# Performance work log

Measured on AMD Instinct MI355X. Metric: run time of the kernel, lower is better.

The kernel has to match this reference:

```python
import jax, jax.numpy as jnp
import numpy as np

N = 100000      # nodes
E = 1600000     # edges (before self-loops)
IN = 128        # in_channels
H = 4           # heads
C = 32          # hidden_channels (per head)
HC = H * C      # 128, LayerNorm dim
NEG_SLOPE = 0.2
LN_EPS = 1e-5


def setup_inputs() -> dict:
    key = jax.random.key(0)
    ks = jax.random.split(key, 8)
    x = jax.random.normal(ks[0], (N, IN), dtype=jnp.float32)
    edge_index = jax.random.randint(ks[1], (2, E), 0, N, dtype=jnp.int64)
    edge_weight = jax.random.uniform(ks[2], (E,), dtype=jnp.float32)
    # GATConv parameters
    W = jax.random.normal(ks[3], (IN, HC), dtype=jnp.float32) * (1.0 / np.sqrt(IN))
    att_src = jax.random.normal(ks[4], (H, C), dtype=jnp.float32) * (1.0 / np.sqrt(C))
    att_dst = jax.random.normal(ks[5], (H, C), dtype=jnp.float32) * (1.0 / np.sqrt(C))
    bias = jnp.zeros((HC,), dtype=jnp.float32)
    # LayerNorm parameters
    gamma = jnp.ones((HC,), dtype=jnp.float32)
    beta = jnp.zeros((HC,), dtype=jnp.float32)
    return {"x": x, "edge_index": edge_index, "edge_weight": edge_weight,
            "W": W, "att_src": att_src, "att_dst": att_dst, "bias": bias,
            "gamma": gamma, "beta": beta}


def reference(x, edge_index, edge_weight, W, att_src, att_dst, bias, gamma, beta):
    # --- GATConv (heads=4, concat, add_self_loops=True) ---
    loops = jnp.arange(N, dtype=edge_index.dtype)
    ei = jnp.concatenate([edge_index, jnp.stack([loops, loops])], axis=1)  # [2, E+N]
    src, dst = ei[0], ei[1]

    xw = (x @ W).reshape(N, H, C)                       # [N, H, C]
    a_src = jnp.sum(xw * att_src, axis=-1)              # [N, H]
    a_dst = jnp.sum(xw * att_dst, axis=-1)              # [N, H]

    # per-edge attention logits, softmax grouped by destination node
    e = jax.nn.leaky_relu(a_src[src] + a_dst[dst], NEG_SLOPE)   # [E+N, H]
    m = jax.ops.segment_max(e, dst, num_segments=N)             # [N, H]
    ex = jnp.exp(e - m[dst])
    denom = jax.ops.segment_sum(ex, dst, num_segments=N)        # [N, H]
    alpha = ex / (denom[dst] + 1e-16)                           # [E+N, H]

    # weighted scatter-add of source features to destinations
    msg = alpha[:, :, None] * xw[src]                           # [E+N, H, C]
    out = jax.ops.segment_sum(msg, dst, num_segments=N)         # [N, H, C]
    out = out.reshape(N, HC) + bias                             # concat heads + bias

    # --- LayerNorm ---
    mu = jnp.mean(out, axis=-1, keepdims=True)
    var = jnp.var(out, axis=-1, keepdims=True)
    return gamma * (out - mu) / jnp.sqrt(var + LN_EPS) + beta
```

## Files before the change

kernel.cpp:

```cpp
#include <hip/hip_runtime.h>
#include <math.h>

#define NN 100000
#define EE 1600000
#define ETOT (EE + NN)
#define NBUK 512
#define NPB 196
#define CHUNK 3125
#define CAP 6144

typedef __attribute__((ext_vector_type(8))) short bf16x8;
typedef __attribute__((ext_vector_type(4))) float f32x4;

__device__ __forceinline__ unsigned short f2bf(float f) {
  unsigned int u = __float_as_uint(f);
  u = u + 0x7fffu + ((u >> 16) & 1u);
  return (unsigned short)(u >> 16);
}

__device__ __forceinline__ float lrelu_exp(float e) {
  e = (e > 0.f) ? e : 0.2f * e;
  return __expf(e);
}

__global__ __launch_bounds__(256) void k_gemm(const float* __restrict__ x,
                                              const float* __restrict__ W,
                                              const float* __restrict__ att_src,
                                              const float* __restrict__ att_dst,
                                              unsigned short* __restrict__ xwb,
                                              float* __restrict__ asrc,
                                              float* __restrict__ adst) {
  __shared__ __align__(16) unsigned short lds[17408];
  __shared__ float satt[256];
  int tid = threadIdx.x;
  for (int i = tid; i < 16384; i += 256) {
    int k = i >> 7, n = i & 127;
    lds[n * 136 + k] = f2bf(W[i]);
  }
  if (tid < 128) satt[tid] = att_src[tid];
  else satt[tid] = att_dst[tid - 128];
  __syncthreads();

  int wv = tid >> 6, lane = tid & 63;
  int m = lane & 15, q = lane >> 4;
  int r = blockIdx.x * 64 + wv * 16 + m;
  bool rok = (r < NN);

  bf16x8 af[4];
#pragma unroll
  for (int kt = 0; kt < 4; kt++) {
    float4 v0 = make_float4(0.f, 0.f, 0.f, 0.f), v1 = v0;
    if (rok) {
      v0 = ((const float4*)x)[(size_t)r * 32 + kt * 8 + q * 2];
      v1 = ((const float4*)x)[(size_t)r * 32 + kt * 8 + q * 2 + 1];
    }
    af[kt][0] = (short)f2bf(v0.x); af[kt][1] = (short)f2bf(v0.y);
    af[kt][2] = (short)f2bf(v0.z); af[kt][3] = (short)f2bf(v0.w);
    af[kt][4] = (short)f2bf(v1.x); af[kt][5] = (short)f2bf(v1.y);
    af[kt][6] = (short)f2bf(v1.z); af[kt][7] = (short)f2bf(v1.w);
  }

  f32x4 acc[8];
#pragma unroll
  for (int nt = 0; nt < 8; nt++) acc[nt] = (f32x4){0.f, 0.f, 0.f, 0.f};

#pragma unroll
  for (int nt = 0; nt < 8; nt++) {
#pragma unroll
    for (int kt = 0; kt < 4; kt++) {
      bf16x8 bf = *((const bf16x8*)&lds[(nt * 16 + m) * 136 + kt * 32 + q * 8]);
      acc[nt] = __builtin_amdgcn_mfma_f32_16x16x32_bf16(af[kt], bf, acc[nt], 0, 0, 0);
    }
  }

  __syncthreads();
#pragma unroll
  for (int nt = 0; nt < 8; nt++)
#pragma unroll
    for (int rg = 0; rg < 4; rg++)
      lds[(wv * 16 + q * 4 + rg) * 128 + nt * 16 + m] = f2bf(acc[nt][rg]);
  __syncthreads();

  size_t base = (size_t)blockIdx.x * 16384;
  const size_t lim = (size_t)NN * 256;
  for (int i = tid; i < 1024; i += 256) {
    size_t off = base + (size_t)i * 16;
    if (off < lim) *((uint4*)((char*)xwb + off)) = ((const uint4*)lds)[i];
  }

  int row = tid >> 2, h = tid & 3;
  int node = blockIdx.x * 64 + row;
  if (node < NN) {
    float ss = 0.f, sd = 0.f;
#pragma unroll
    for (int cq = 0; cq < 4; cq++) {
      uint4 u = *((const uint4*)&lds[row * 128 + h * 32 + cq * 8]);
      int cb = h * 32 + cq * 8;
      float f0 = __uint_as_float(u.x << 16), f1 = __uint_as_float(u.x & 0xffff0000u);
      float f2 = __uint_as_float(u.y << 16), f3 = __uint_as_float(u.y & 0xffff0000u);
      float f4 = __uint_as_float(u.z << 16), f5 = __uint_as_float(u.z & 0xffff0000u);
      float f6 = __uint_as_float(u.w << 16), f7 = __uint_as_float(u.w & 0xffff0000u);
      ss += f0 * satt[cb] + f1 * satt[cb + 1] + f2 * satt[cb + 2] + f3 * satt[cb + 3] +
            f4 * satt[cb + 4] + f5 * satt[cb + 5] + f6 * satt[cb + 6] + f7 * satt[cb + 7];
      sd += f0 * satt[128 + cb] + f1 * satt[128 + cb + 1] + f2 * satt[128 + cb + 2] +
            f3 * satt[128 + cb + 3] + f4 * satt[128 + cb + 4] + f5 * satt[128 + cb + 5] +
            f6 * satt[128 + cb + 6] + f7 * satt[128 + cb + 7];
    }
    asrc[(size_t)node * 4 + h] = ss;
    adst[(size_t)node * 4 + h] = sd;
  }
}

__global__ __launch_bounds__(256) void k_p1(const int* __restrict__ ei,
                                            int* __restrict__ H) {
  __shared__ int h[NBUK];
  int j = blockIdx.x, t = threadIdx.x;
  for (int i = t; i < NBUK; i += 256) h[i] = 0;
  __syncthreads();
  int e0 = j * CHUNK;
  for (int e = e0 + t; e < e0 + CHUNK; e += 256) {
    int d = ei[(size_t)EE + e];
    atomicAdd(&h[d / NPB], 1);
  }
  __syncthreads();
  for (int i = t; i < NBUK; i += 256) H[j * NBUK + i] = h[i];
}

__global__ __launch_bounds__(512) void k_s1(const int* __restrict__ H,
                                            int* __restrict__ R, int* __restrict__ T) {
  __shared__ int s[512];
  int b = blockIdx.x, t = threadIdx.x;
  int v = H[t * NBUK + b];
  s[t] = v;
  __syncthreads();
  for (int off = 1; off < 512; off <<= 1) {
    int tmp = (t >= off) ? s[t - off] : 0;
    __syncthreads();
    s[t] += tmp;
    __syncthreads();
  }
  R[b * 512 + t] = s[t] - v;
  if (t == 511) T[b] = s[511];
}

__global__ __launch_bounds__(512) void k_s2(const int* __restrict__ T,
                                            int* __restrict__ BaseTmp,
                                            int* __restrict__ Base) {
  __shared__ int s[512];
  __shared__ int s2[512];
  int t = threadIdx.x;
  int v = T[t];
  int ncnt = NN - t * NPB;
  ncnt = (ncnt < 0) ? 0 : ((ncnt > NPB) ? NPB : ncnt);
  int w = v + ncnt;
  s[t] = v; s2[t] = w;
  __syncthreads();
  for (int off = 1; off < 512; off <<= 1) {
    int ta = (t >= off) ? s[t - off] : 0;
    int tb = (t >= off) ? s2[t - off] : 0;
    __syncthreads();
    s[t] += ta; s2[t] += tb;
    __syncthreads();
  }
  BaseTmp[t] = s[t] - v;
  Base[t] = s2[t] - w;
}

__global__ __launch_bounds__(256) void k_p3(const int* __restrict__ ei,
                                            const int* __restrict__ R,
                                            const int* __restrict__ BaseTmp,
                                            int* __restrict__ tmpb) {
  __shared__ int cur[NBUK];
  int j = blockIdx.x, t = threadIdx.x;
  for (int b = t; b < NBUK; b += 256) cur[b] = BaseTmp[b] + R[b * 512 + j];
  __syncthreads();
  int e0 = j * CHUNK;
  for (int e = e0 + t; e < e0 + CHUNK; e += 256) {
    int s = ei[e];
    int d = ei[(size_t)EE + e];
    int b = d / NPB;
    int li = d - b * NPB;
    int pos = atomicAdd(&cur[b], 1);
    tmpb[pos] = (li << 17) | s;
  }
}

__global__ __launch_bounds__(256) void k_p4(const int* __restrict__ tmpb,
                                            const int* __restrict__ T,
                                            const int* __restrict__ BaseTmp,
                                            const int* __restrict__ Base,
                                            const float* __restrict__ asrc,
                                            const float* __restrict__ adst,
                                            int* __restrict__ es, int* __restrict__ offs,
                                            float* __restrict__ na) {
  __shared__ int cnt[256];
  __shared__ int cur[NPB];
  __shared__ int stage[CAP];
  __shared__ __align__(16) float ssum[NPB * 4];
  __shared__ __align__(16) float adl[NPB * 4];
  int b = blockIdx.x, t = threadIdx.x;
  if (b == 0 && t == 0) offs[NN] = ETOT;
  int n0 = b * NPB;
  int nloc = NN - n0;
  if (nloc <= 0) return;
  if (nloc > NPB) nloc = NPB;
  int total = T[b];
  int bt = BaseTmp[b], bs = Base[b];
  cnt[t] = (t < nloc) ? 1 : 0;
  for (int i = t; i < NPB * 4; i += 256) ssum[i] = 0.f;
  for (int i = t; i < nloc * 4; i += 256) adl[i] = adst[(size_t)n0 * 4 + i];
  __syncthreads();
  for (int e = t; e < total; e += 256) {
    int u = tmpb[bt + e];
    atomicAdd(&cnt[u >> 17], 1);
  }
  __syncthreads();
  int v = cnt[t];
  __syncthreads();
  for (int off = 1; off < 256; off <<= 1) {
    int tmp = (t >= off) ? cnt[t - off] : 0;
    __syncthreads();
    cnt[t] += tmp;
    __syncthreads();
  }
  int excl = cnt[t] - v;
  if (t < nloc) {
    int node = n0 + t;
    offs[node] = bs + excl;
    cur[t] = excl + 1;
    if (excl < CAP) {
      stage[excl] = node;
      float4 asv = *((const float4*)(asrc + (size_t)node * 4));
      float4 adv = *((const float4*)&adl[t * 4]);
      float4 w4;
      w4.x = lrelu_exp(asv.x + adv.x); w4.y = lrelu_exp(asv.y + adv.y);
      w4.z = lrelu_exp(asv.z + adv.z); w4.w = lrelu_exp(asv.w + adv.w);
      atomicAdd(&ssum[t * 4 + 0], w4.x); atomicAdd(&ssum[t * 4 + 1], w4.y);
      atomicAdd(&ssum[t * 4 + 2], w4.z); atomicAdd(&ssum[t * 4 + 3], w4.w);
    }
  }
  __syncthreads();
  for (int e = t; e < total; e += 256) {
    int u = tmpb[bt + e];
    int li = u >> 17;
    int src = u & 0x1FFFF;
    int pos = atomicAdd(&cur[li], 1);
    if (pos < CAP) {
      stage[pos] = src;
      float4 asv = *((const float4*)(asrc + (size_t)src * 4));
      float4 adv = *((const float4*)&adl[li * 4]);
      float4 w4;
      w4.x = lrelu_exp(asv.x + adv.x); w4.y = lrelu_exp(asv.y + adv.y);
      w4.z = lrelu_exp(asv.z + adv.z); w4.w = lrelu_exp(asv.w + adv.w);
      atomicAdd(&ssum[li * 4 + 0], w4.x); atomicAdd(&ssum[li * 4 + 1], w4.y);
      atomicAdd(&ssum[li * 4 + 2], w4.z); atomicAdd(&ssum[li * 4 + 3], w4.w);
    }
  }
  __syncthreads();
  int btot = total + nloc;
  if (btot > CAP) btot = CAP;
  for (int i = t; i < btot; i += 256) es[bs + i] = stage[i];
  for (int i = t; i < nloc * 4; i += 256)
    na[(size_t)n0 * 4 + i] = 1.f / (ssum[i] + 1e-16f);
}

__global__ __launch_bounds__(256) void k_agg(const unsigned short* __restrict__ xwb,
                                             const float* __restrict__ asrc,
                                             const float* __restrict__ adst,
                                             const float* __restrict__ na,
                                             const int* __restrict__ offs,
                                             const int* __restrict__ es,
                                             const float* __restrict__ bias,
                                             const float* __restrict__ gamma,
                                             const float* __restrict__ beta,
                                             float* __restrict__ out) {
  int lane = threadIdx.x & 63;
  int node = blockIdx.x * 4 + (threadIdx.x >> 6);
  int off0 = offs[node];
  int d = offs[node + 1] - off0;
  int h = lane >> 4;
  int c = lane * 2;
  float rn = na[(size_t)node * 4 + h];
  float ad = adst[(size_t)node * 4 + h];

  const unsigned* xp = (const unsigned*)xwb + lane;
  const int* ep = es + off0;
  float ax0 = 0.f, ay0 = 0.f, ax1 = 0.f, ay1 = 0.f;

  int j = 0;
  for (; j + 8 <= d; j += 8) {
    int4 sa = *((const int4*)(ep + j));
    int4 sb = *((const int4*)(ep + j + 4));
    int sv[8] = {sa.x, sa.y, sa.z, sa.w, sb.x, sb.y, sb.z, sb.w};
    float av[8];
    unsigned uu[8];
#pragma unroll
    for (int q = 0; q < 8; q++) {
      av[q] = asrc[(size_t)(unsigned)sv[q] * 4 + h];
      uu[q] = xp[(unsigned)sv[q] * 64u];
    }
#pragma unroll
    for (int q = 0; q < 8; q++) {
      float w = lrelu_exp(av[q] + ad);
      float lo = __uint_as_float(uu[q] << 16);
      float hi = __uint_as_float(uu[q] & 0xffff0000u);
      if (q & 1) { ax1 = fmaf(w, lo, ax1); ay1 = fmaf(w, hi, ay1); }
      else       { ax0 = fmaf(w, lo, ax0); ay0 = fmaf(w, hi, ay0); }
    }
  }
  for (; j < d; ++j) {
    int s0 = ep[j];
    float w = lrelu_exp(asrc[(size_t)(unsigned)s0 * 4 + h] + ad);
    unsigned u0 = xp[(unsigned)s0 * 64u];
    ax0 = fmaf(w, __uint_as_float(u0 << 16), ax0);
    ay0 = fmaf(w, __uint_as_float(u0 & 0xffff0000u), ay0);
  }
  float accx = ax0 + ax1, accy = ay0 + ay1;

  float vx = accx * rn + bias[c];
  float vy = accy * rn + bias[c + 1];
  float sum = vx + vy, sq = vx * vx + vy * vy;
#pragma unroll
  for (int o = 32; o; o >>= 1) {
    sum += __shfl_xor(sum, o);
    sq += __shfl_xor(sq, o);
  }
  float mean = sum * (1.f / 128.f);
  float var = sq * (1.f / 128.f) - mean * mean;
  float rs = rsqrtf(var + 1e-5f);
  float o0 = gamma[c] * (vx - mean) * rs + beta[c];
  float o1 = gamma[c + 1] * (vy - mean) * rs + beta[c + 1];
  float2 ov; ov.x = o0; ov.y = o1;
  *((float2*)(out + (size_t)node * 128 + c)) = ov;
}

extern "C" void kernel_launch(void* const* d_in, const int* in_sizes, int n_in,
                              void* d_out, int out_size, void* d_ws, size_t ws_size,
                              hipStream_t stream) {
  const float* x = (const float*)d_in[0];
  const int* ei = (const int*)d_in[1];
  const float* W = (const float*)d_in[3];
  const float* att_src = (const float*)d_in[4];
  const float* att_dst = (const float*)d_in[5];
  const float* bias = (const float*)d_in[6];
  const float* gamma = (const float*)d_in[7];
  const float* beta = (const float*)d_in[8];
  float* out = (float*)d_out;

  char* p = (char*)d_ws;
  auto alloc = [&](size_t bytes) -> char* {
    char* r = p;
    p += (bytes + 255) & ~(size_t)255;
    return r;
  };
  unsigned short* xwb = (unsigned short*)alloc((size_t)NN * 128 * 2);
  float* asrc = (float*)alloc((size_t)NN * 4 * 4);
  float* adst = (float*)alloc((size_t)NN * 4 * 4);
  int* es = (int*)alloc((size_t)ETOT * 4);
  int* offs = (int*)alloc((size_t)(NN + 1) * 4);
  float* na = (float*)alloc((size_t)NN * 4 * 4);
  int* tmpb = (int*)alloc((size_t)EE * 4);
  int* H = (int*)alloc((size_t)512 * NBUK * 4);
  int* R = (int*)alloc((size_t)NBUK * 512 * 4);
  int* T = (int*)alloc((size_t)NBUK * 4);
  int* BaseTmp = (int*)alloc((size_t)(NBUK + 1) * 4);
  int* Base = (int*)alloc((size_t)(NBUK + 1) * 4);

  k_gemm<<<(NN + 63) / 64, 256, 0, stream>>>(x, W, att_src, att_dst, xwb, asrc, adst);
  k_p1<<<512, 256, 0, stream>>>(ei, H);
  k_s1<<<NBUK, 512, 0, stream>>>(H, R, T);
  k_s2<<<1, 512, 0, stream>>>(T, BaseTmp, Base);
  k_p3<<<512, 256, 0, stream>>>(ei, R, BaseTmp, tmpb);
  k_p4<<<NBUK, 256, 0, stream>>>(tmpb, T, BaseTmp, Base, asrc, adst, es, offs, na);
  k_agg<<<NN / 4, 256, 0, stream>>>(xwb, asrc, adst, na, offs, es, bias, gamma, beta, out);
}
```

Baseline: 302.6 us.

## Fuse softmax denominator into aggregation and compute edge weights once per lane

The per-destination softmax denominator is no longer computed in the CSR build kernel (k_p4) with shared-memory float atomics. Instead, k_agg accumulates the sum of weights alongside the weighted features and normalises at the end. Inside the 8-edge loop, each lane now computes one (edge, head) exponential and broadcasts it with shuffles, rather than every lane recomputing exp for all 8 edges. This removes the asrc gathers, the exps and the atomics from k_p4, plus the na buffer round trip, in exchange for extra shuffles and a running sum in the aggregation kernel.

After: 270.6 us. 10.6% less time.

```diff
diff --git a/kernel.cpp b/kernel.cpp
--- a/kernel.cpp
+++ b/kernel.cpp
@@ -189,15 +189,10 @@
                                             const int* __restrict__ T,
                                             const int* __restrict__ BaseTmp,
                                             const int* __restrict__ Base,
-                                            const float* __restrict__ asrc,
-                                            const float* __restrict__ adst,
-                                            int* __restrict__ es, int* __restrict__ offs,
-                                            float* __restrict__ na) {
+                                            int* __restrict__ es, int* __restrict__ offs) {
   __shared__ int cnt[256];
   __shared__ int cur[NPB];
   __shared__ int stage[CAP];
-  __shared__ __align__(16) float ssum[NPB * 4];
-  __shared__ __align__(16) float adl[NPB * 4];
   int b = blockIdx.x, t = threadIdx.x;
   if (b == 0 && t == 0) offs[NN] = ETOT;
   int n0 = b * NPB;
@@ -207,8 +202,6 @@
   int total = T[b];
   int bt = BaseTmp[b], bs = Base[b];
   cnt[t] = (t < nloc) ? 1 : 0;
-  for (int i = t; i < NPB * 4; i += 256) ssum[i] = 0.f;
-  for (int i = t; i < nloc * 4; i += 256) adl[i] = adst[(size_t)n0 * 4 + i];
   __syncthreads();
   for (int e = t; e < total; e += 256) {
     int u = tmpb[bt + e];
@@ -225,49 +218,25 @@
   }
   int excl = cnt[t] - v;
   if (t < nloc) {
-    int node = n0 + t;
-    offs[node] = bs + excl;
+    offs[n0 + t] = bs + excl;
     cur[t] = excl + 1;
-    if (excl < CAP) {
-      stage[excl] = node;
-      float4 asv = *((const float4*)(asrc + (size_t)node * 4));
-      float4 adv = *((const float4*)&adl[t * 4]);
-      float4 w4;
-      w4.x = lrelu_exp(asv.x + adv.x); w4.y = lrelu_exp(asv.y + adv.y);
-      w4.z = lrelu_exp(asv.z + adv.z); w4.w = lrelu_exp(asv.w + adv.w);
-      atomicAdd(&ssum[t * 4 + 0], w4.x); atomicAdd(&ssum[t * 4 + 1], w4.y);
-      atomicAdd(&ssum[t * 4 + 2], w4.z); atomicAdd(&ssum[t * 4 + 3], w4.w);
-    }
+    if (excl < CAP) stage[excl] = n0 + t;
   }
   __syncthreads();
   for (int e = t; e < total; e += 256) {
     int u = tmpb[bt + e];
-    int li = u >> 17;
-    int src = u & 0x1FFFF;
-    int pos = atomicAdd(&cur[li], 1);
-    if (pos < CAP) {
-      stage[pos] = src;
-      float4 asv = *((const float4*)(asrc + (size_t)src * 4));
-      float4 adv = *((const float4*)&adl[li * 4]);
-      float4 w4;
-      w4.x = lrelu_exp(asv.x + adv.x); w4.y = lrelu_exp(asv.y + adv.y);
-      w4.z = lrelu_exp(asv.z + adv.z); w4.w = lrelu_exp(asv.w + adv.w);
-      atomicAdd(&ssum[li * 4 + 0], w4.x); atomicAdd(&ssum[li * 4 + 1], w4.y);
-      atomicAdd(&ssum[li * 4 + 2], w4.z); atomicAdd(&ssum[li * 4 + 3], w4.w);
-    }
+    int pos = atomicAdd(&cur[u >> 17], 1);
+    if (pos < CAP) stage[pos] = u & 0x1FFFF;
   }
   __syncthreads();
   int btot = total + nloc;
   if (btot > CAP) btot = CAP;
   for (int i = t; i < btot; i += 256) es[bs + i] = stage[i];
-  for (int i = t; i < nloc * 4; i += 256)
-    na[(size_t)n0 * 4 + i] = 1.f / (ssum[i] + 1e-16f);
 }
 
 __global__ __launch_bounds__(256) void k_agg(const unsigned short* __restrict__ xwb,
                                              const float* __restrict__ asrc,
                                              const float* __restrict__ adst,
-                                             const float* __restrict__ na,
                                              const int* __restrict__ offs,
                                              const int* __restrict__ es,
                                              const float* __restrict__ bias,
@@ -279,43 +248,69 @@
   int off0 = offs[node];
   int d = offs[node + 1] - off0;
   int h = lane >> 4;
+  int he = lane & 3;
   int c = lane * 2;
-  float rn = na[(size_t)node * 4 + h];
-  float ad = adst[(size_t)node * 4 + h];
+
+  float4 ad4 = *((const float4*)(adst + (size_t)node * 4));
+  float adh = (h & 2) ? ((h & 1) ? ad4.w : ad4.z) : ((h & 1) ? ad4.y : ad4.x);
+  float ade = (he & 2) ? ((he & 1) ? ad4.w : ad4.z) : ((he & 1) ? ad4.y : ad4.x);
 
   const unsigned* xp = (const unsigned*)xwb + lane;
   const int* ep = es + off0;
   float ax0 = 0.f, ay0 = 0.f, ax1 = 0.f, ay1 = 0.f;
+  float wsum = 0.f;
 
   int j = 0;
   for (; j + 8 <= d; j += 8) {
     int4 sa = *((const int4*)(ep + j));
     int4 sb = *((const int4*)(ep + j + 4));
-    int sv[8] = {sa.x, sa.y, sa.z, sa.w, sb.x, sb.y, sb.z, sb.w};
-    float av[8];
-    unsigned uu[8];
-#pragma unroll
-    for (int q = 0; q < 8; q++) {
-      av[q] = asrc[(size_t)(unsigned)sv[q] * 4 + h];
-      uu[q] = xp[(unsigned)sv[q] * 64u];
-    }
-#pragma unroll
-    for (int q = 0; q < 8; q++) {
-      float w = lrelu_exp(av[q] + ad);
-      float lo = __uint_as_float(uu[q] << 16);
-      float hi = __uint_as_float(uu[q] & 0xffff0000u);
-      if (q & 1) { ax1 = fmaf(w, lo, ax1); ay1 = fmaf(w, hi, ay1); }
-      else       { ax0 = fmaf(w, lo, ax0); ay0 = fmaf(w, hi, ay0); }
-    }
+    int se = ep[j + (lane >> 3)];
+    float av = asrc[(size_t)(unsigned)se * 4u + (unsigned)he];
+    unsigned u0 = xp[(unsigned)sa.x * 64u];
+    unsigned u1 = xp[(unsigned)sa.y * 64u];
+    unsigned u2 = xp[(unsigned)sa.z * 64u];
+    unsigned u3 = xp[(unsigned)sa.w * 64u];
+    unsigned u4 = xp[(unsigned)sb.x * 64u];
+    unsigned u5 = xp[(unsigned)sb.y * 64u];
+    unsigned u6 = xp[(unsigned)sb.z * 64u];
+    unsigned u7 = xp[(unsigned)sb.w * 64u];
+    float wl = lrelu_exp(av + ade);
+    float w0 = __shfl(wl, 0 * 8 + h);
+    float w1 = __shfl(wl, 1 * 8 + h);
+    float w2 = __shfl(wl, 2 * 8 + h);
+    float w3 = __shfl(wl, 3 * 8 + h);
+    float w4 = __shfl(wl, 4 * 8 + h);
+    float w5 = __shfl(wl, 5 * 8 + h);
+    float w6 = __shfl(wl, 6 * 8 + h);
+    float w7 = __shfl(wl, 7 * 8 + h);
+    wsum += ((w0 + w1) + (w2 + w3)) + ((w4 + w5) + (w6 + w7));
+    ax0 = fmaf(w0, __uint_as_float(u0 << 16), ax0);
+    ay0 = fmaf(w0, __uint_as_float(u0 & 0xffff0000u), ay0);
+    ax1 = fmaf(w1, __uint_as_float(u1 << 16), ax1);
+    ay1 = fmaf(w1, __uint_as_float(u1 & 0xffff0000u), ay1);
+    ax0 = fmaf(w2, __uint_as_float(u2 << 16), ax0);
+    ay0 = fmaf(w2, __uint_as_float(u2 & 0xffff0000u), ay0);
+    ax1 = fmaf(w3, __uint_as_float(u3 << 16), ax1);
+    ay1 = fmaf(w3, __uint_as_float(u3 & 0xffff0000u), ay1);
+    ax0 = fmaf(w4, __uint_as_float(u4 << 16), ax0);
+    ay0 = fmaf(w4, __uint_as_float(u4 & 0xffff0000u), ay0);
+    ax1 = fmaf(w5, __uint_as_float(u5 << 16), ax1);
+    ay1 = fmaf(w5, __uint_as_float(u5 & 0xffff0000u), ay1);
+    ax0 = fmaf(w6, __uint_as_float(u6 << 16), ax0);
+    ay0 = fmaf(w6, __uint_as_float(u6 & 0xffff0000u), ay0);
+    ax1 = fmaf(w7, __uint_as_float(u7 << 16), ax1);
+    ay1 = fmaf(w7, __uint_as_float(u7 & 0xffff0000u), ay1);
   }
   for (; j < d; ++j) {
     int s0 = ep[j];
-    float w = lrelu_exp(asrc[(size_t)(unsigned)s0 * 4 + h] + ad);
+    float w = lrelu_exp(asrc[(size_t)(unsigned)s0 * 4u + (unsigned)h] + adh);
+    wsum += w;
     unsigned u0 = xp[(unsigned)s0 * 64u];
     ax0 = fmaf(w, __uint_as_float(u0 << 16), ax0);
     ay0 = fmaf(w, __uint_as_float(u0 & 0xffff0000u), ay0);
   }
   float accx = ax0 + ax1, accy = ay0 + ay1;
+  float rn = 1.f / (wsum + 1e-16f);
 
   float vx = accx * rn + bias[c];
   float vy = accy * rn + bias[c + 1];
@@ -358,7 +353,6 @@
   float* adst = (float*)alloc((size_t)NN * 4 * 4);
   int* es = (int*)alloc((size_t)ETOT * 4);
   int* offs = (int*)alloc((size_t)(NN + 1) * 4);
-  float* na = (float*)alloc((size_t)NN * 4 * 4);
   int* tmpb = (int*)alloc((size_t)EE * 4);
   int* H = (int*)alloc((size_t)512 * NBUK * 4);
   int* R = (int*)alloc((size_t)NBUK * 512 * 4);
@@ -371,6 +365,6 @@
   k_s1<<<NBUK, 512, 0, stream>>>(H, R, T);
   k_s2<<<1, 512, 0, stream>>>(T, BaseTmp, Base);
   k_p3<<<512, 256, 0, stream>>>(ei, R, BaseTmp, tmpb);
-  k_p4<<<NBUK, 256, 0, stream>>>(tmpb, T, BaseTmp, Base, asrc, adst, es, offs, na);
-  k_agg<<<NN / 4, 256, 0, stream>>>(xwb, asrc, adst, na, offs, es, bias, gamma, beta, out);
-}
+  k_p4<<<NBUK, 256, 0, stream>>>(tmpb, T, BaseTmp, Base, es, offs);
+  k_agg<<<NN / 4, 256, 0, stream>>>(xwb, asrc, adst, offs, es, bias, gamma, beta, out);
+}
```
